# Kernel optimization log

Hardware: AMD Instinct MI355X
Metric: run time of the kernel (lower is better)

Reference implementation:

```python
import jax, jax.numpy as jnp
import numpy as np

N_EMBED = 1024
HEAD_SIZE = 128
B, T = 4, 2048

def setup_inputs() -> dict:
    key = jax.random.key(0)
    kx, kq, kk, kv = jax.random.split(key, 4)
    bound = 1.0 / np.sqrt(N_EMBED)  # torch Linear default init range
    x = jax.random.normal(kx, (B, T, N_EMBED), dtype=jnp.float32)
    Wq = jax.random.uniform(kq, (N_EMBED, HEAD_SIZE), jnp.float32, -bound, bound)
    Wk = jax.random.uniform(kk, (N_EMBED, HEAD_SIZE), jnp.float32, -bound, bound)
    Wv = jax.random.uniform(kv, (N_EMBED, HEAD_SIZE), jnp.float32, -bound, bound)
    return {"x": x, "Wq": Wq, "Wk": Wk, "Wv": Wv}

def reference(x, Wq, Wk, Wv):
    Bn, Tn, C = x.shape
    q = x @ Wq  # [B,T,H]
    k = x @ Wk
    v = x @ Wv
    # NOTE: original scales by C**-0.5 where C = n_embed (not head_size)
    scale = C ** (-0.5)
    wei = jnp.einsum('bqh,bkh->bqk', q, k) * scale  # [B,T,T]
    causal = jnp.tril(jnp.ones((Tn, Tn), dtype=bool))
    wei = jnp.where(causal, wei, -jnp.inf)
    wei = jax.nn.softmax(wei, axis=-1)
    # dropout p=0.0 -> identity
    return jnp.einsum('bqk,bkh->bqh', wei, v)
```

## Files before the change

kernel.cpp:

```cpp
#include <hip/hip_runtime.h>
#include <stdint.h>

#define B_ 4
#define T_ 2048
#define C_ 1024
#define H_ 128
#define NEG_BIG -3.0e38f

typedef __attribute__((ext_vector_type(8))) short short8;
typedef __attribute__((ext_vector_type(4))) float f32x4;
typedef __attribute__((ext_vector_type(4))) unsigned short ushort4v;
typedef __attribute__((ext_vector_type(8))) unsigned short ushort8v;

__device__ __forceinline__ unsigned short f2bf(float f) {
  union { float f; unsigned u; } cv; cv.f = f;
  return (unsigned short)((cv.u + 0x8000u) >> 16);
}

__device__ __forceinline__ float bf2f(unsigned short s) {
  union { unsigned u; float f; } cv; cv.u = ((unsigned)s) << 16;
  return cv.f;
}

__device__ __forceinline__ void gld16(const void* g, void* l) {
  __builtin_amdgcn_global_load_lds(
      (const __attribute__((address_space(1))) unsigned int*)g,
      (__attribute__((address_space(3))) unsigned int*)l, 16, 0, 0);
}

#define CSCALE 0.045084220027780106f

__global__ __launch_bounds__(256, 3) void qkv_proj(const float* __restrict__ x,
                                                   const float* __restrict__ Wq,
                                                   const float* __restrict__ Wk,
                                                   const float* __restrict__ Wv,
                                                   unsigned short* __restrict__ Qb,
                                                   unsigned short* __restrict__ Kb,
                                                   unsigned short* __restrict__ VT) {
  __shared__ unsigned short As[2][64 * 64];
  __shared__ unsigned short Bs[2][64 * 64];

  const int tid  = threadIdx.x;
  const int wave = tid >> 6, lane = tid & 63;
  const int quad = lane >> 4, l15 = lane & 15;
  const int rb = blockIdx.x & 127, cb = blockIdx.x >> 7;
  const int gm0 = rb * 64, gn0 = cb * 64;
  const int wm = wave >> 1, wn = wave & 1;

  const int bn = tid & 63, bkc = tid >> 6;
  const float* Wsrc = (cb < 2) ? Wq : (cb < 4) ? Wk : Wv;
  const int bh = (gn0 & 127) + bn;

  const int axr = tid >> 3, axc = tid & 7;
  const float* gAx = x + (size_t)(gm0 + axr) * C_ + axc * 8;

  int aoff[2][2], boff[2][2];
#pragma unroll
  for (int mt = 0; mt < 2; ++mt) {
    const int r = wm * 32 + mt * 16 + l15;
#pragma unroll
    for (int ks = 0; ks < 2; ++ks)
      aoff[mt][ks] = r * 64 + (((ks * 4 + quad) ^ r) & 7) * 8;
  }
#pragma unroll
  for (int nt = 0; nt < 2; ++nt) {
    const int r = wn * 32 + nt * 16 + l15;
#pragma unroll
    for (int ks = 0; ks < 2; ++ks)
      boff[nt][ks] = r * 64 + ((((ks * 4 + quad)) ^ r ^ (r >> 3)) & 7) * 8;
  }

  f32x4 acc[2][2];
  const f32x4 zero4 = {0.f, 0.f, 0.f, 0.f};
#pragma unroll
  for (int mt = 0; mt < 2; ++mt)
#pragma unroll
    for (int nt = 0; nt < 2; ++nt) acc[mt][nt] = zero4;

#define LOAD_B(ko_)                                                                \
  _Pragma("unroll")                                                                \
  for (int kk = 0; kk < 16; ++kk)                                                  \
    bv[kk] = Wsrc[(size_t)((ko_) + bkc * 16 + kk) * 128 + bh];

#define WRITE_B(buf)                                                               \
  {                                                                                \
    short8 bw0, bw1;                                                               \
    _Pragma("unroll")                                                              \
    for (int e = 0; e < 8; ++e) {                                                  \
      bw0[e] = (short)f2bf(bv[e]);                                                 \
      bw1[e] = (short)f2bf(bv[8 + e]);                                             \
    }                                                                              \
    const int sx = bn ^ (bn >> 3);                                                 \
    *(short8*)(&Bs[buf][bn * 64 + (((bkc * 2) ^ sx) & 7) * 8]) = bw0;              \
    *(short8*)(&Bs[buf][bn * 64 + (((bkc * 2 + 1) ^ sx) & 7) * 8]) = bw1;          \
  }

#define LOAD_A(ko_)                                                                \
  _Pragma("unroll")                                                                \
  for (int q = 0; q < 2; ++q) {                                                    \
    av0[q] = *(const f32x4*)(gAx + (size_t)(q * 32) * C_ + (ko_));                 \
    av1[q] = *(const f32x4*)(gAx + (size_t)(q * 32) * C_ + (ko_) + 4);             \
  }

#define WRITE_A(buf)                                                               \
  _Pragma("unroll")                                                                \
  for (int q = 0; q < 2; ++q) {                                                    \
    const int row = axr + q * 32;                                                  \
    short8 aw;                                                                     \
    _Pragma("unroll")                                                              \
    for (int e = 0; e < 4; ++e) {                                                  \
      aw[e]     = (short)f2bf(av0[q][e]);                                          \
      aw[4 + e] = (short)f2bf(av1[q][e]);                                          \
    }                                                                              \
    *(short8*)(&As[buf][row * 64 + ((axc ^ row) & 7) * 8]) = aw;                   \
  }

  f32x4 av0[2], av1[2];
  float bv[16];
  LOAD_A(0);
  LOAD_B(0);
  WRITE_A(0);
  WRITE_B(0);

  for (int kb = 0; kb < 16; ++kb) {
    __syncthreads();
    const int cur = kb & 1, nxt = cur ^ 1;
    if (kb + 1 < 16) {
      LOAD_A((kb + 1) * 64);
      LOAD_B((kb + 1) * 64);
    }
    const unsigned short* Ac = As[cur];
    const unsigned short* Bc = Bs[cur];
#pragma unroll
    for (int ks = 0; ks < 2; ++ks) {
      short8 b0 = *(const short8*)(Bc + boff[0][ks]);
      short8 b1 = *(const short8*)(Bc + boff[1][ks]);
#pragma unroll
      for (int mt = 0; mt < 2; ++mt) {
        short8 a = *(const short8*)(Ac + aoff[mt][ks]);
        acc[mt][0] = __builtin_amdgcn_mfma_f32_16x16x32_bf16(a, b0, acc[mt][0], 0, 0, 0);
        acc[mt][1] = __builtin_amdgcn_mfma_f32_16x16x32_bf16(a, b1, acc[mt][1], 0, 0, 0);
      }
    }
    if (kb + 1 < 16) {
      WRITE_A(nxt);
      WRITE_B(nxt);
    }
  }
#undef LOAD_B
#undef WRITE_B
#undef LOAD_A
#undef WRITE_A

#pragma unroll
  for (int mt = 0; mt < 2; ++mt) {
    const int row0 = gm0 + wm * 32 + mt * 16 + quad * 4;
#pragma unroll
    for (int nt = 0; nt < 2; ++nt) {
      const int colbase = gn0 + wn * 32 + nt * 16;
      const int col = colbase + l15;
      if (colbase < 128) {
#pragma unroll
        for (int r = 0; r < 4; ++r)
          Qb[(size_t)(row0 + r) * H_ + col] = f2bf(acc[mt][nt][r] * CSCALE);
      } else if (colbase < 256) {
#pragma unroll
        for (int r = 0; r < 4; ++r)
          Kb[(size_t)(row0 + r) * H_ + (col - 128)] = f2bf(acc[mt][nt][r]);
      } else {
        const int h = col - 256;
        const int bidx = row0 >> 11;
        const int t0 = row0 & 2047;
        ushort4v pk;
        pk[0] = f2bf(acc[mt][nt][0]); pk[1] = f2bf(acc[mt][nt][1]);
        pk[2] = f2bf(acc[mt][nt][2]); pk[3] = f2bf(acc[mt][nt][3]);
        *(ushort4v*)(VT + (size_t)(bidx * H_ + h) * T_ + t0) = pk;
      }
    }
  }
}

__global__ __launch_bounds__(256, 2) void attn1(const unsigned short* __restrict__ Qb,
                                                const unsigned short* __restrict__ Kb,
                                                const unsigned short* __restrict__ VT,
                                                unsigned short* __restrict__ Opart,
                                                float* __restrict__ mpart,
                                                float* __restrict__ lpart) {
  __shared__ unsigned short Ks[2][64 * 128];
  __shared__ unsigned short Vs[2][128 * 64];
  __shared__ unsigned short Pls[4][16 * 72];

  const int bid = blockIdx.x;
  const int b  = bid & 3;
  const int jp = (bid >> 2) & 15;
  const int ch = bid >> 6;
  const int j1 = jp, j2 = 31 - jp;
  const int n1 = (ch <= j1) ? (((j1 - ch) >> 3) + 1) : 0;
  const int n2 = ((j2 - ch) >> 3) + 1;
  const int ntt = n1 + n2;

  const int tid  = threadIdx.x;
  const int wave = tid >> 6, lane = tid & 63;
  const int quad = lane >> 4, l15 = lane & 15;

  const unsigned short* Kb_b = Kb + (size_t)(b * T_) * H_;
  const unsigned short* VT_b = VT + (size_t)(b * H_) * T_;

  const int k_row4 = lane >> 4, k_slot = lane & 15;
  const int v_row8 = lane >> 3, v_slot = lane & 7;

#define STAGE_KV(buf, kv0_)                                                        \
  {                                                                                \
    _Pragma("unroll")                                                              \
    for (int i_ = 0; i_ < 4; ++i_) {                                               \
      const int r = wave * 16 + i_ * 4 + k_row4;                                   \
      const int c2 = (k_slot & 8) | ((k_slot ^ r) & 7);                            \
      gld16(Kb_b + (size_t)((kv0_) + r) * H_ + c2 * 8,                             \
            &Ks[buf][(wave * 16 + i_ * 4) * 128]);                                 \
    }                                                                              \
    _Pragma("unroll")                                                              \
    for (int i_ = 0; i_ < 4; ++i_) {                                               \
      const int h = wave * 32 + i_ * 8 + v_row8;                                   \
      gld16(VT_b + (size_t)h * T_ + (kv0_) + ((v_slot ^ h) & 7) * 8,               \
            &Vs[buf][(wave * 32 + i_ * 8) * 64]);                                  \
    }                                                                              \
  }

#define EPI(jr_)                                                                   \
  {                                                                                \
    const int pid = (b * 32 + (jr_)) * 8 + ch;                                     \
    unsigned short* po = Opart + (size_t)(pid * 64 + wave * 16) * H_;              \
    _Pragma("unroll")                                                              \
    for (int nth = 0; nth < 8; ++nth)                                              \
      _Pragma("unroll")                                                            \
      for (int r = 0; r < 4; ++r)                                                  \
        po[(quad * 4 + r) * H_ + nth * 16 + l15] = f2bf(O[nth][r]);                \
    if (lane < 16) {                                                               \
      mpart[pid * 64 + wave * 16 + lane] = m_;                                     \
      lpart[pid * 64 + wave * 16 + lane] = l_;                                     \
    }                                                                              \
  }

  int jr_cur = n1 ? j1 : j2;
  short8 aq[4];
  {
    const unsigned short* qrow = Qb + (size_t)(b * T_ + jr_cur * 64 + wave * 16 + l15) * H_;
#pragma unroll
    for (int ks = 0; ks < 4; ++ks)
      aq[ks] = *(const short8*)(qrow + ks * 32 + quad * 8);
  }

  STAGE_KV(0, ch * 64);

  const f32x4 zero4 = {0.f, 0.f, 0.f, 0.f};
  f32x4 O[8];
#pragma unroll
  for (int nth = 0; nth < 8; ++nth) O[nth] = zero4;
  float m_ = NEG_BIG, l_ = 0.f;

  for (int i = 0; i < ntt; ++i) {
    __syncthreads();
    if (i + 1 < ntt) {
      const int in_ = i + 1;
      const int tn = (in_ < n1) ? (ch + (in_ << 3)) : (ch + ((in_ - n1) << 3));
      STAGE_KV((in_) & 1, tn * 64);
    }
    if (n1 && i == n1) {
      EPI(j1);
      m_ = NEG_BIG; l_ = 0.f;
#pragma unroll
      for (int nth = 0; nth < 8; ++nth) O[nth] = zero4;
      jr_cur = j2;
      const unsigned short* qrow = Qb + (size_t)(b * T_ + j2 * 64 + wave * 16 + l15) * H_;
#pragma unroll
      for (int ks = 0; ks < 4; ++ks)
        aq[ks] = *(const short8*)(qrow + ks * 32 + quad * 8);
    }
    const int ti  = (i < n1) ? (ch + (i << 3)) : (ch + ((i - n1) << 3));
    const int kv0 = ti * 64;

    const unsigned short* kb = Ks[i & 1];
    f32x4 ST[4];
    ST[0] = zero4; ST[1] = zero4; ST[2] = zero4; ST[3] = zero4;
    __builtin_amdgcn_s_setprio(1);
#pragma unroll
    for (int ntl = 0; ntl < 4; ++ntl) {
      const int kvr = ntl * 16 + l15;
#pragma unroll
      for (int ks = 0; ks < 4; ++ks) {
        const int c = ks * 4 + quad;
        const int slot = (c & 8) | ((c ^ kvr) & 7);
        short8 kf = *(const short8*)(kb + kvr * 128 + slot * 8);
        ST[ntl] = __builtin_amdgcn_mfma_f32_16x16x32_bf16(kf, aq[ks], ST[ntl], 0, 0, 0);
      }
    }
    __builtin_amdgcn_s_setprio(0);

    if (ti == jr_cur) {
      const int ql = jr_cur * 64 + wave * 16 + l15;
#pragma unroll
      for (int ntl = 0; ntl < 4; ++ntl)
#pragma unroll
        for (int r = 0; r < 4; ++r) {
          const int kl = kv0 + ntl * 16 + quad * 4 + r;
          if (kl > ql) ST[ntl][r] = NEG_BIG;
        }
    }

    float pmax = ST[0][0];
#pragma unroll
    for (int ntl = 0; ntl < 4; ++ntl)
#pragma unroll
      for (int r = 0; r < 4; ++r) pmax = fmaxf(pmax, ST[ntl][r]);
    pmax = fmaxf(pmax, __shfl_xor(pmax, 16));
    pmax = fmaxf(pmax, __shfl_xor(pmax, 32));
    if (!__all(pmax <= m_ + 8.f)) {
      const float mn = fmaxf(m_, pmax);
      const float alpha = __builtin_amdgcn_exp2f(m_ - mn);
      m_ = mn;
      l_ *= alpha;
      float alr[4];
#pragma unroll
      for (int r = 0; r < 4; ++r) alr[r] = __shfl(alpha, quad * 4 + r);
#pragma unroll
      for (int nth = 0; nth < 8; ++nth)
#pragma unroll
        for (int r = 0; r < 4; ++r) O[nth][r] *= alr[r];
    }
    float s = 0.f;
#pragma unroll
    for (int ntl = 0; ntl < 4; ++ntl)
#pragma unroll
      for (int r = 0; r < 4; ++r) {
        const float p = __builtin_amdgcn_exp2f(ST[ntl][r] - m_);
        ST[ntl][r] = p;
        s += p;
      }
    s += __shfl_xor(s, 16);
    s += __shfl_xor(s, 32);
    l_ += s;

#pragma unroll
    for (int ntl = 0; ntl < 4; ++ntl) {
      ushort4v pk;
      pk[0] = f2bf(ST[ntl][0]); pk[1] = f2bf(ST[ntl][1]);
      pk[2] = f2bf(ST[ntl][2]); pk[3] = f2bf(ST[ntl][3]);
      *(ushort4v*)(&Pls[wave][l15 * 72 + ntl * 16 + quad * 4]) = pk;
    }

    const unsigned short* vb = Vs[i & 1];
    short8 ap0 = *(const short8*)(&Pls[wave][l15 * 72 + quad * 8]);
    short8 ap1 = *(const short8*)(&Pls[wave][l15 * 72 + 32 + quad * 8]);
    __builtin_amdgcn_s_setprio(1);
#pragma unroll
    for (int nth = 0; nth < 8; ++nth) {
      const int h = nth * 16 + l15;
      short8 v0 = *(const short8*)(vb + h * 64 + ((quad ^ h) & 7) * 8);
      short8 v1 = *(const short8*)(vb + h * 64 + (((4 + quad) ^ h) & 7) * 8);
      O[nth] = __builtin_amdgcn_mfma_f32_16x16x32_bf16(ap0, v0, O[nth], 0, 0, 0);
      O[nth] = __builtin_amdgcn_mfma_f32_16x16x32_bf16(ap1, v1, O[nth], 0, 0, 0);
    }
    __builtin_amdgcn_s_setprio(0);
  }
  EPI(j2);
#undef STAGE_KV
#undef EPI
}

__global__ __launch_bounds__(256) void attn2(const unsigned short* __restrict__ Opart,
                                             const float* __restrict__ mpart,
                                             const float* __restrict__ lpart,
                                             float* __restrict__ out) {
  const int b = blockIdx.x & 3;
  const int j = (blockIdx.x >> 2) & 31;
  const int qi = blockIdx.x >> 7;
  const int nch = min(j + 1, 8);
  const int tid = threadIdx.x;
  const int q = (tid >> 4) + qi * 16;
  const int h0 = (tid & 15) * 8;
  const int pbase = (b * 32 + j) * 8;

  float m_fin = NEG_BIG;
  for (int ch = 0; ch < nch; ++ch)
    m_fin = fmaxf(m_fin, mpart[(pbase + ch) * 64 + q]);
  float lf = 0.f;
  float o[8];
#pragma unroll
  for (int c = 0; c < 8; ++c) o[c] = 0.f;
  for (int ch = 0; ch < nch; ++ch) {
    const int pid = pbase + ch;
    const float sc = __builtin_amdgcn_exp2f(mpart[pid * 64 + q] - m_fin);
    lf += sc * lpart[pid * 64 + q];
    ushort8v pv = *(const ushort8v*)(Opart + (size_t)(pid * 64 + q) * H_ + h0);
#pragma unroll
    for (int c = 0; c < 8; ++c) o[c] += sc * bf2f(pv[c]);
  }
  const float inv = 1.0f / lf;
  float* op = out + (size_t)(b * T_ + j * 64 + q) * H_ + h0;
  f32x4 v0 = {o[0] * inv, o[1] * inv, o[2] * inv, o[3] * inv};
  f32x4 v1 = {o[4] * inv, o[5] * inv, o[6] * inv, o[7] * inv};
  *(f32x4*)(op) = v0;
  *(f32x4*)(op + 4) = v1;
}

extern "C" void kernel_launch(void* const* d_in, const int* in_sizes, int n_in,
                              void* d_out, int out_size, void* d_ws, size_t ws_size,
                              hipStream_t stream) {
  const float* x  = (const float*)d_in[0];
  const float* Wq = (const float*)d_in[1];
  const float* Wk = (const float*)d_in[2];
  const float* Wv = (const float*)d_in[3];
  float* out = (float*)d_out;

  char* ws = (char*)d_ws;
  unsigned short* Qb  = (unsigned short*)(ws + 1048576);
  unsigned short* Kb  = (unsigned short*)(ws + 3145728);
  unsigned short* VT  = (unsigned short*)(ws + 5242880);
  unsigned short* Opart = (unsigned short*)(ws + 8388608);
  float* mpart = (float*)(ws + 25165824);
  float* lpart = (float*)(ws + 25427968);

  qkv_proj<<<dim3(768), dim3(256), 0, stream>>>(x, Wq, Wk, Wv, Qb, Kb, VT);
  attn1<<<dim3(512), dim3(256), 0, stream>>>(Qb, Kb, VT, Opart, mpart, lpart);
  attn2<<<dim3(512), dim3(256), 0, stream>>>(Opart, mpart, lpart, out);
}
```

Measured before the change: 116.0 us.

## Replace LDS double buffering with register-staged single buffer and 3-block occupancy

Swaps the double-buffered async global-to-LDS staging of K/V tiles for a scheme that loads the next tile into registers, then writes it to a single LDS buffer after the current tile's compute. This halves the K/V shared memory, and the launch bound is raised from 2 to 3 blocks per CU. The goal is more concurrent waves to hide latency. The cost is higher register pressure from the staging registers and two barriers per iteration, and the write to LDS is now serialized after compute.

```diff
diff --git a/kernel.cpp b/kernel.cpp
--- a/kernel.cpp
+++ b/kernel.cpp
@@ -180,14 +180,14 @@
   }
 }
 
-__global__ __launch_bounds__(256, 2) void attn1(const unsigned short* __restrict__ Qb,
+__global__ __launch_bounds__(256, 3) void attn1(const unsigned short* __restrict__ Qb,
                                                 const unsigned short* __restrict__ Kb,
                                                 const unsigned short* __restrict__ VT,
                                                 unsigned short* __restrict__ Opart,
                                                 float* __restrict__ mpart,
                                                 float* __restrict__ lpart) {
-  __shared__ unsigned short Ks[2][64 * 128];
-  __shared__ unsigned short Vs[2][128 * 64];
+  __shared__ unsigned short Ks[64 * 128];
+  __shared__ unsigned short Vs[128 * 64];
   __shared__ unsigned short Pls[4][16 * 72];
 
   const int bid = blockIdx.x;
@@ -209,20 +209,36 @@
   const int k_row4 = lane >> 4, k_slot = lane & 15;
   const int v_row8 = lane >> 3, v_slot = lane & 7;
 
-#define STAGE_KV(buf, kv0_)                                                        \
+  f32x4 kreg[4], vreg[4];
+
+#define TILE(i_) (((i_) < n1) ? (ch + ((i_) << 3)) : (ch + (((i_) - n1) << 3)))
+
+#define LOAD_KV(kv0_)                                                              \
   {                                                                                \
     _Pragma("unroll")                                                              \
     for (int i_ = 0; i_ < 4; ++i_) {                                               \
       const int r = wave * 16 + i_ * 4 + k_row4;                                   \
       const int c2 = (k_slot & 8) | ((k_slot ^ r) & 7);                            \
-      gld16(Kb_b + (size_t)((kv0_) + r) * H_ + c2 * 8,                             \
-            &Ks[buf][(wave * 16 + i_ * 4) * 128]);                                 \
+      kreg[i_] = *(const f32x4*)(Kb_b + (size_t)((kv0_) + r) * H_ + c2 * 8);       \
     }                                                                              \
     _Pragma("unroll")                                                              \
     for (int i_ = 0; i_ < 4; ++i_) {                                               \
       const int h = wave * 32 + i_ * 8 + v_row8;                                   \
-      gld16(VT_b + (size_t)h * T_ + (kv0_) + ((v_slot ^ h) & 7) * 8,               \
-            &Vs[buf][(wave * 32 + i_ * 8) * 64]);                                  \
+      vreg[i_] = *(const f32x4*)(VT_b + (size_t)h * T_ + (kv0_) + ((v_slot ^ h) & 7) * 8); \
+    }                                                                              \
+  }
+
+#define WRITE_KV()                                                                 \
+  {                                                                                \
+    _Pragma("unroll")                                                              \
+    for (int i_ = 0; i_ < 4; ++i_) {                                               \
+      const int r = wave * 16 + i_ * 4 + k_row4;                                   \
+      *(f32x4*)(&Ks[r * 128 + k_slot * 8]) = kreg[i_];                             \
+    }                                                                              \
+    _Pragma("unroll")                                                              \
+    for (int i_ = 0; i_ < 4; ++i_) {                                               \
+      const int h = wave * 32 + i_ * 8 + v_row8;                                   \
+      *(f32x4*)(&Vs[h * 64 + v_slot * 8]) = vreg[i_];                              \
     }                                                                              \
   }
 
@@ -250,7 +266,10 @@
       aq[ks] = *(const short8*)(qrow + ks * 32 + quad * 8);
   }
 
-  STAGE_KV(0, ch * 64);
+  LOAD_KV(TILE(0) * 64);
+  WRITE_KV();
+  LOAD_KV(TILE(1) * 64);
+  __syncthreads();
 
   const f32x4 zero4 = {0.f, 0.f, 0.f, 0.f};
   f32x4 O[8];
@@ -259,12 +278,6 @@
   float m_ = NEG_BIG, l_ = 0.f;
 
   for (int i = 0; i < ntt; ++i) {
-    __syncthreads();
-    if (i + 1 < ntt) {
-      const int in_ = i + 1;
-      const int tn = (in_ < n1) ? (ch + (in_ << 3)) : (ch + ((in_ - n1) << 3));
-      STAGE_KV((in_) & 1, tn * 64);
-    }
     if (n1 && i == n1) {
       EPI(j1);
       m_ = NEG_BIG; l_ = 0.f;
@@ -276,10 +289,9 @@
       for (int ks = 0; ks < 4; ++ks)
         aq[ks] = *(const short8*)(qrow + ks * 32 + quad * 8);
     }
-    const int ti  = (i < n1) ? (ch + (i << 3)) : (ch + ((i - n1) << 3));
+    const int ti  = TILE(i);
     const int kv0 = ti * 64;
 
-    const unsigned short* kb = Ks[i & 1];
     f32x4 ST[4];
     ST[0] = zero4; ST[1] = zero4; ST[2] = zero4; ST[3] = zero4;
     __builtin_amdgcn_s_setprio(1);
@@ -290,7 +302,7 @@
       for (int ks = 0; ks < 4; ++ks) {
         const int c = ks * 4 + quad;
         const int slot = (c & 8) | ((c ^ kvr) & 7);
-        short8 kf = *(const short8*)(kb + kvr * 128 + slot * 8);
+        short8 kf = *(const short8*)(Ks + kvr * 128 + slot * 8);
         ST[ntl] = __builtin_amdgcn_mfma_f32_16x16x32_bf16(kf, aq[ks], ST[ntl], 0, 0, 0);
       }
     }
@@ -348,22 +360,30 @@
       *(ushort4v*)(&Pls[wave][l15 * 72 + ntl * 16 + quad * 4]) = pk;
     }
 
-    const unsigned short* vb = Vs[i & 1];
     short8 ap0 = *(const short8*)(&Pls[wave][l15 * 72 + quad * 8]);
     short8 ap1 = *(const short8*)(&Pls[wave][l15 * 72 + 32 + quad * 8]);
     __builtin_amdgcn_s_setprio(1);
 #pragma unroll
     for (int nth = 0; nth < 8; ++nth) {
       const int h = nth * 16 + l15;
-      short8 v0 = *(const short8*)(vb + h * 64 + ((quad ^ h) & 7) * 8);
-      short8 v1 = *(const short8*)(vb + h * 64 + (((4 + quad) ^ h) & 7) * 8);
+      short8 v0 = *(const short8*)(Vs + h * 64 + ((quad ^ h) & 7) * 8);
+      short8 v1 = *(const short8*)(Vs + h * 64 + (((4 + quad) ^ h) & 7) * 8);
       O[nth] = __builtin_amdgcn_mfma_f32_16x16x32_bf16(ap0, v0, O[nth], 0, 0, 0);
       O[nth] = __builtin_amdgcn_mfma_f32_16x16x32_bf16(ap1, v1, O[nth], 0, 0, 0);
     }
     __builtin_amdgcn_s_setprio(0);
+
+    if (i + 1 < ntt) {
+      __syncthreads();
+      WRITE_KV();
+      if (i + 2 < ntt) LOAD_KV(TILE(i + 2) * 64);
+      __syncthreads();
+    }
   }
   EPI(j2);
-#undef STAGE_KV
+#undef TILE
+#undef LOAD_KV
+#undef WRITE_KV
 #undef EPI
 }
 
```

After: 115.9 us. No clear change (-0.1%).
